# Kernel optimization log

Hardware: AMD Instinct MI355X
Metric: run time of the kernel (lower is better)

Reference implementation:

```python
import jax, jax.numpy as jnp
import numpy as np

D_MODEL, D_HEAD, N_HEAD, PERIOD = 1024, 64, 16, 30
B, T1, T2 = 2, 2048, 2048


def setup_inputs() -> dict:
    key = jax.random.key(0)
    ks = jax.random.split(key, 7)
    s_in = 1.0 / np.sqrt(D_MODEL)
    s_out = 1.0 / np.sqrt(N_HEAD * D_HEAD)
    return {
        "x": jax.random.normal(ks[0], (B, T1, D_MODEL), dtype=jnp.float32),
        "context": jax.random.normal(ks[1], (B, T2, D_MODEL), dtype=jnp.float32),
        "Wq": jax.random.uniform(ks[2], (N_HEAD * D_HEAD, D_MODEL), jnp.float32, -s_in, s_in),
        "Wk": jax.random.uniform(ks[3], (N_HEAD * D_HEAD, D_MODEL), jnp.float32, -s_in, s_in),
        "Wv": jax.random.uniform(ks[4], (N_HEAD * D_HEAD, D_MODEL), jnp.float32, -s_in, s_in),
        "Wo": jax.random.uniform(ks[5], (D_MODEL, N_HEAD * D_HEAD), jnp.float32, -s_out, s_out),
        "bo": jax.random.uniform(ks[6], (D_MODEL,), jnp.float32, -s_out, s_out),
    }


def reference(x, context, Wq, Wk, Wv, Wo, bo):
    Bx, T1x, _ = x.shape
    T2x = context.shape[1]
    scale = 1.0 / np.sqrt(D_HEAD).astype(np.float32)
    # projections (torch Linear: y = x @ W^T)
    q = (x @ Wq.T).reshape(Bx, T1x, N_HEAD, D_HEAD)
    k = (context @ Wk.T).reshape(Bx, T2x, N_HEAD, D_HEAD)
    v = (context @ Wv.T).reshape(Bx, T2x, N_HEAD, D_HEAD)
    # attention scores [B, H, T1, T2]
    scores = jnp.einsum('bihd,bjhd->bhij', q, k) * scale
    # ALiBi-style periodic distance bias
    dist = jnp.abs(jnp.arange(T1x)[:, None] - jnp.arange(T2x)[None, :])  # [T1,T2]
    bias = -(dist // PERIOD).astype(jnp.float32)                          # [T1,T2]
    head_scale = jnp.power(2.0, -jnp.arange(1, N_HEAD + 1, dtype=jnp.float32))
    biased = scores + bias[None, None, :, :] * head_scale[None, :, None, None]
    attn = jax.nn.softmax(biased, axis=-1)
    out = jnp.einsum('bhij,bjhd->bihd', attn, v).reshape(Bx, T1x, N_HEAD * D_HEAD)
    # output projection; dropout is identity in eval mode
    return out @ Wo.T + bo
```

## Files before the change

kernel.cpp:

```cpp
#include <hip/hip_runtime.h>
#include <hip/hip_fp16.h>

typedef _Float16 f16;
typedef __attribute__((ext_vector_type(8))) _Float16 f16x8;
typedef __attribute__((ext_vector_type(4))) _Float16 f16x4;
typedef __attribute__((ext_vector_type(2))) __fp16 fp16x2;
typedef __attribute__((ext_vector_type(4))) float f32x4;

#define DM 1024
#define NH 16
#define DH 64
#define TT 2048
#define LOG2E 1.4426950408889634f
#define QSCALE 0.18033688f

__device__ __forceinline__ void gl16(const void* g, void* l) {
  __builtin_amdgcn_global_load_lds((const __attribute__((address_space(1))) void*)g,
                                   (__attribute__((address_space(3))) void*)l, 16, 0, 0);
}

__global__ __launch_bounds__(256) void cvt_all(const float* __restrict__ x, const float* __restrict__ cx,
                                               const float* __restrict__ wq, const float* __restrict__ wk,
                                               const float* __restrict__ wv, const float* __restrict__ wo,
                                               f16* __restrict__ xb, f16* __restrict__ cb,
                                               f16* __restrict__ wqb, f16* __restrict__ wkb,
                                               f16* __restrict__ wvb, f16* __restrict__ wob) {
  int idx = blockIdx.x * 256 + threadIdx.x;
  int stride = gridDim.x * 256;
  for (int i = idx; i < 3145728; i += stride) {
    const float* src; f16* dst; int off; float s = 1.0f;
    if (i < 2097152) {
      if (i < 1048576) { src = x; dst = xb; off = i; }
      else { src = cx; dst = cb; off = i - 1048576; }
    } else {
      int j = i - 2097152;
      int wsel = j >> 18;
      off = j & 262143;
      if (wsel == 0) { src = wq; dst = wqb; s = QSCALE; }
      else if (wsel == 1) { src = wk; dst = wkb; }
      else if (wsel == 2) { src = wv; dst = wvb; }
      else { src = wo; dst = wob; }
    }
    float4 v = reinterpret_cast<const float4*>(src)[off];
    f16x4 o = { (f16)(v.x * s), (f16)(v.y * s), (f16)(v.z * s), (f16)(v.w * s) };
    reinterpret_cast<f16x4*>(dst)[off] = o;
  }
}

__global__ __launch_bounds__(256) void fbgen(f16* __restrict__ FB) {
  int i = blockIdx.x;
  int j0 = threadIdx.x * 8;
  f16x8 v;
#pragma unroll
  for (int e = 0; e < 8; e++) {
    int d = i - (j0 + e); d = (d < 0) ? -d : d;
    v[e] = (f16)(d / 30);
  }
  *reinterpret_cast<f16x8*>(&FB[(size_t)i * TT + j0]) = v;
}

__device__ __forceinline__ void gemm_mainloop(const f16* __restrict__ A, const f16* __restrict__ W,
                                              int bm, int bn, f16 (*As)[4096], f16 (*Bs)[4096],
                                              f32x4 (&acc)[4][4]) {
  int t = threadIdx.x;
  int w = t >> 6;
  int lane = t & 63, lr = lane & 15, g = lane >> 4;
  int wr = w >> 1, wc = w & 1;
  int scol = ((t & 3) ^ ((t >> 3) & 3)) * 8;
  const f16* a0 = A + (size_t)(bm + (t >> 2)) * DM + scol;
  const f16* b0 = W + (size_t)(bn + (t >> 2)) * DM + scol;
  int wo = w * 512;
  int szg = ((lr >> 1) & 3) << 4;

  auto STG = [&](int bufi, int kt) {
    gl16(a0 + kt, As[bufi] + wo);
    gl16(a0 + kt + (size_t)64 * DM, As[bufi] + 2048 + wo);
    gl16(b0 + kt, Bs[bufi] + wo);
    gl16(b0 + kt + (size_t)64 * DM, Bs[bufi] + 2048 + wo);
  };

  STG(0, 0);
  __syncthreads();
  int buf = 0;
  for (int kt = 0; kt < DM; kt += 32) {
    if (kt + 32 < DM) STG(buf ^ 1, kt + 32);
    const char* Ab = (const char*)As[buf];
    const char* Bb = (const char*)Bs[buf];
    f16x8 af[4], bf[4];
#pragma unroll
    for (int mi = 0; mi < 4; mi++) {
      int row = wr * 64 + mi * 16 + lr;
      af[mi] = *reinterpret_cast<const f16x8*>(Ab + row * 64 + ((g << 4) ^ szg));
    }
#pragma unroll
    for (int ni = 0; ni < 4; ni++) {
      int row = wc * 64 + ni * 16 + lr;
      bf[ni] = *reinterpret_cast<const f16x8*>(Bb + row * 64 + ((g << 4) ^ szg));
    }
    __builtin_amdgcn_s_setprio(1);
#pragma unroll
    for (int mi = 0; mi < 4; mi++)
#pragma unroll
      for (int ni = 0; ni < 4; ni++)
        acc[mi][ni] = __builtin_amdgcn_mfma_f32_16x16x32_f16(af[mi], bf[ni], acc[mi][ni], 0, 0, 0);
    __builtin_amdgcn_s_setprio(0);
    __syncthreads();
    buf ^= 1;
  }
}

__global__ __launch_bounds__(256) void qkv_gemm(const f16* __restrict__ xb, const f16* __restrict__ cb,
                                                const f16* __restrict__ wq, const f16* __restrict__ wk,
                                                const f16* __restrict__ wv,
                                                f16* __restrict__ Qo, f16* __restrict__ Ko,
                                                f16* __restrict__ Vt) {
  __shared__ f16 As[2][4096];
  __shared__ f16 Bs[2][4096];
  int gid = blockIdx.x >> 8;
  int bid = blockIdx.x & 255;
  int bm = (bid >> 3) * 128, bn = (bid & 7) * 128;
  const f16* A = (gid == 0) ? xb : cb;
  const f16* W = (gid == 0) ? wq : ((gid == 1) ? wk : wv);
  f32x4 acc[4][4] = {};
  gemm_mainloop(A, W, bm, bn, As, Bs, acc);

  int t = threadIdx.x, w = t >> 6, lane = t & 63, lr = lane & 15, g = lane >> 4;
  int wr = w >> 1, wc = w & 1;
  if (gid < 2) {
    f16* out = (gid == 0) ? Qo : Ko;
#pragma unroll
    for (int mi = 0; mi < 4; mi++) {
      int m0 = bm + wr * 64 + mi * 16 + 4 * g;
      int b = m0 >> 11, i0 = m0 & 2047;
#pragma unroll
      for (int ni = 0; ni < 4; ni++) {
        int n = bn + wc * 64 + ni * 16 + lr;
        int h = n >> 6, d = n & 63;
        size_t base = (((size_t)(b * NH + h)) * TT + i0) * DH + d;
#pragma unroll
        for (int r = 0; r < 4; r++)
          out[base + (size_t)r * DH] = (f16)acc[mi][ni][r];
      }
    }
  } else {
#pragma unroll
    for (int mi = 0; mi < 4; mi++) {
      int m0 = bm + wr * 64 + mi * 16 + 4 * g;
      int b = m0 >> 11, j0 = m0 & 2047;
#pragma unroll
      for (int ni = 0; ni < 4; ni++) {
        int n = bn + wc * 64 + ni * 16 + lr;
        int h = n >> 6, d = n & 63;
        f16x4 pk = { (f16)acc[mi][ni][0], (f16)acc[mi][ni][1],
                     (f16)acc[mi][ni][2], (f16)acc[mi][ni][3] };
        *reinterpret_cast<f16x4*>(&Vt[(((size_t)(b * NH + h)) * DH + d) * TT + j0]) = pk;
      }
    }
  }
}

__global__ __launch_bounds__(256) void out_gemm(const f16* __restrict__ Ob, const f16* __restrict__ wo,
                                                const float* __restrict__ bo, float* __restrict__ Y) {
  __shared__ f16 As[2][4096];
  __shared__ f16 Bs[2][4096];
  int bid = blockIdx.x;
  int bm = (bid >> 3) * 128, bn = (bid & 7) * 128;
  f32x4 acc[4][4] = {};
  gemm_mainloop(Ob, wo, bm, bn, As, Bs, acc);
  int t = threadIdx.x, w = t >> 6, lane = t & 63, lr = lane & 15, g = lane >> 4;
  int wr = w >> 1, wc = w & 1;
#pragma unroll
  for (int mi = 0; mi < 4; mi++) {
    int m0 = bm + wr * 64 + mi * 16 + 4 * g;
#pragma unroll
    for (int ni = 0; ni < 4; ni++) {
      int n = bn + wc * 64 + ni * 16 + lr;
      float bias = bo[n];
#pragma unroll
      for (int r = 0; r < 4; r++)
        Y[(size_t)(m0 + r) * DM + n] = acc[mi][ni][r] + bias;
    }
  }
}

__global__ __launch_bounds__(256, 4) void attn_kernel(const f16* __restrict__ Q, const f16* __restrict__ K,
                                                      const f16* __restrict__ V, const f16* __restrict__ FB,
                                                      f16* __restrict__ O) {
  __shared__ f16 KV[2][8192];
  int o = blockIdx.x;
  int bid = (((o & 7) << 2) + (o >> 8)) * 32 + ((o >> 3) & 31);
  int qt = bid & 31, bh = bid >> 5, h = bh & 15, b = bh >> 4;
  int t = threadIdx.x, w = t >> 6, lane = t & 63, lr = lane & 15, g = lane >> 4;
  int qw = qt * 64 + w * 16;
  int qi = qw + lr;

  const f16* qrow = Q + ((size_t)bh * TT + qi) * DH + g * 8;
  f16x8 qf0 = *reinterpret_cast<const f16x8*>(qrow);
  f16x8 qf1 = *reinterpret_cast<const f16x8*>(qrow + 32);

  const float nc2 = -exp2f(-(float)(h + 1)) * LOG2E;
  f32x4 rsv = { 0.f, 0.f, 0.f, 0.f };
  f32x4 oacc[4] = {};

  const f16* fbrow = FB + (size_t)qi * TT + (g << 3);

  int srow = w * 8 + (lane >> 3);
  int gr = lane & 7;
  int sw = gr ^ ((srow & 3) | ((srow & 8) >> 1));
  const f16* ksrc = K + ((size_t)bh * TT + srow) * DH + sw * 8;
  const f16* vsrc = V + ((size_t)bh * DH + srow) * TT + sw * 8;
  int wo = w * 512;

  auto STG = [&](int bufi, int kv0) {
    f16* base = KV[bufi];
    gl16(ksrc + (size_t)kv0 * DH, base + wo);
    gl16(ksrc + (size_t)(kv0 + 32) * DH, base + 2048 + wo);
    gl16(vsrc + kv0, base + 4096 + wo);
    gl16(vsrc + (size_t)32 * TT + kv0, base + 6144 + wo);
  };

  int jp = ((lr >> 2) << 3) + (lr & 3);
  int szk = ((lr & 3) | (((lr >> 2) & 1) << 2)) << 4;
  int szv = ((lr & 3) | ((lr & 8) >> 1)) << 4;

  STG(0, 0);
  __syncthreads();
  int buf = 0;

  for (int kv0 = 0; kv0 < TT; kv0 += 64) {
    if (kv0 + 64 < TT) STG(buf ^ 1, kv0 + 64);
    f16x8 fbv0 = *reinterpret_cast<const f16x8*>(fbrow + kv0);
    f16x8 fbv1 = *reinterpret_cast<const f16x8*>(fbrow + kv0 + 32);

    const char* Kb = (const char*)KV[buf];
    const char* Vb = Kb + 8192;

    f32x4 sv[4];
    __builtin_amdgcn_s_setprio(1);
#pragma unroll
    for (int ct = 0; ct < 4; ct++) {
      int jrow = jp + ((ct >> 1) << 5) + ((ct & 1) << 2);
      const char* krow = Kb + jrow * 128;
      f16x8 kb0 = *reinterpret_cast<const f16x8*>(krow + ((g << 4) ^ szk));
      f16x8 kb1 = *reinterpret_cast<const f16x8*>(krow + (((g + 4) << 4) ^ szk));
      f32x4 z = {0.f, 0.f, 0.f, 0.f};
      z = __builtin_amdgcn_mfma_f32_16x16x32_f16(kb0, qf0, z, 0, 0, 0);
      z = __builtin_amdgcn_mfma_f32_16x16x32_f16(kb1, qf1, z, 0, 0, 0);
      sv[ct] = z;
    }
    __builtin_amdgcn_s_setprio(0);

#pragma unroll
    for (int ct = 0; ct < 4; ct++) {
      int e0 = (ct & 1) << 2;
      f32x4 p;
#pragma unroll
      for (int r = 0; r < 4; r++) {
        float fbf = (ct < 2) ? (float)fbv0[e0 + r] : (float)fbv1[e0 + r];
        float sx = fmaf(fbf, nc2, sv[ct][r]);
        p[r] = __builtin_amdgcn_exp2f(sx);
      }
      sv[ct] = p;
      rsv += p;
    }

#pragma unroll
    for (int ks = 0; ks < 2; ks++) {
      union { f16x8 v; fp16x2 hh[4]; } pu;
      pu.hh[0] = __builtin_amdgcn_cvt_pkrtz(sv[2 * ks][0], sv[2 * ks][1]);
      pu.hh[1] = __builtin_amdgcn_cvt_pkrtz(sv[2 * ks][2], sv[2 * ks][3]);
      pu.hh[2] = __builtin_amdgcn_cvt_pkrtz(sv[2 * ks + 1][0], sv[2 * ks + 1][1]);
      pu.hh[3] = __builtin_amdgcn_cvt_pkrtz(sv[2 * ks + 1][2], sv[2 * ks + 1][3]);
      __builtin_amdgcn_s_setprio(1);
#pragma unroll
      for (int dt = 0; dt < 4; dt++) {
        int vr = dt * 16 + lr;
        f16x8 va = *reinterpret_cast<const f16x8*>(Vb + vr * 128 + ((((ks * 4 + g)) << 4) ^ szv));
        oacc[dt] = __builtin_amdgcn_mfma_f32_16x16x32_f16(va, pu.v, oacc[dt], 0, 0, 0);
      }
      __builtin_amdgcn_s_setprio(0);
    }
    __syncthreads();
    buf ^= 1;
  }

  float lsum = (rsv[0] + rsv[1]) + (rsv[2] + rsv[3]);
  lsum += __shfl_xor(lsum, 16, 64);
  lsum += __shfl_xor(lsum, 32, 64);
  float inv = __builtin_amdgcn_rcpf(lsum);
  size_t ob = ((size_t)b * TT + qi) * DM + h * DH + (g << 2);
#pragma unroll
  for (int dt = 0; dt < 4; dt++) {
    f16x4 o4 = { (f16)(oacc[dt][0] * inv), (f16)(oacc[dt][1] * inv),
                 (f16)(oacc[dt][2] * inv), (f16)(oacc[dt][3] * inv) };
    *reinterpret_cast<f16x4*>(&O[ob + dt * 16]) = o4;
  }
}

extern "C" void kernel_launch(void* const* d_in, const int* in_sizes, int n_in,
                              void* d_out, int out_size, void* d_ws, size_t ws_size,
                              hipStream_t stream) {
  const float* x  = (const float*)d_in[0];
  const float* cx = (const float*)d_in[1];
  const float* Wq = (const float*)d_in[2];
  const float* Wk = (const float*)d_in[3];
  const float* Wv = (const float*)d_in[4];
  const float* Wo = (const float*)d_in[5];
  const float* bo = (const float*)d_in[6];
  float* Y = (float*)d_out;

  const size_t NTOK = (size_t)2 * TT;
  f16* p = (f16*)d_ws;
  f16* xb  = p; p += NTOK * DM;
  f16* cb  = p; p += NTOK * DM;
  f16* wqb = p; p += (size_t)DM * DM;
  f16* wkb = p; p += (size_t)DM * DM;
  f16* wvb = p; p += (size_t)DM * DM;
  f16* wob = p; p += (size_t)DM * DM;
  f16* Qb  = p; p += NTOK * DM;
  f16* Kb  = p; p += NTOK * DM;
  f16* Vtb = p; p += NTOK * DM;
  f16* Ob  = p; p += NTOK * DM;
  f16* FBt = xb;

  cvt_all<<<2048, 256, 0, stream>>>(x, cx, Wq, Wk, Wv, Wo, xb, cb, wqb, wkb, wvb, wob);
  qkv_gemm<<<768, 256, 0, stream>>>(xb, cb, wqb, wkb, wvb, Qb, Kb, Vtb);
  fbgen<<<TT, 256, 0, stream>>>(FBt);
  attn_kernel<<<1024, 256, 0, stream>>>(Qb, Kb, Vtb, FBt, Ob);
  out_gemm<<<256, 256, 0, stream>>>(Ob, wob, bo, Y);
}
```

Before: 136.9 us.

## Switch attention to 32x32x16 MFMA with 128-query tiles per block

Rewrites the attention kernel to use 32x32x16 MFMA instructions instead of 16x16x32. Each wave now owns 32 queries and each block 128, so the grid is halved and every staged K/V tile is reused by twice as many queries. The LDS read swizzle and the staging row mapping are redone to match the new fragment layout, and launch bounds drop to 2 blocks per CU. Larger accumulators raise register pressure and lower occupancy, and the fewer blocks may fill the CUs less evenly.

```diff
diff --git a/kernel.cpp b/kernel.cpp
--- a/kernel.cpp
+++ b/kernel.cpp
@@ -6,6 +6,7 @@
 typedef __attribute__((ext_vector_type(4))) _Float16 f16x4;
 typedef __attribute__((ext_vector_type(2))) __fp16 fp16x2;
 typedef __attribute__((ext_vector_type(4))) float f32x4;
+typedef __attribute__((ext_vector_type(16))) float f32x16;
 
 #define DM 1024
 #define NH 16
@@ -183,32 +184,36 @@
   }
 }
 
-__global__ __launch_bounds__(256, 4) void attn_kernel(const f16* __restrict__ Q, const f16* __restrict__ K,
+__global__ __launch_bounds__(256, 2) void attn_kernel(const f16* __restrict__ Q, const f16* __restrict__ K,
                                                       const f16* __restrict__ V, const f16* __restrict__ FB,
                                                       f16* __restrict__ O) {
   __shared__ f16 KV[2][8192];
   int o = blockIdx.x;
-  int bid = (((o & 7) << 2) + (o >> 8)) * 32 + ((o >> 3) & 31);
-  int qt = bid & 31, bh = bid >> 5, h = bh & 15, b = bh >> 4;
-  int t = threadIdx.x, w = t >> 6, lane = t & 63, lr = lane & 15, g = lane >> 4;
-  int qw = qt * 64 + w * 16;
-  int qi = qw + lr;
-
-  const f16* qrow = Q + ((size_t)bh * TT + qi) * DH + g * 8;
-  f16x8 qf0 = *reinterpret_cast<const f16x8*>(qrow);
-  f16x8 qf1 = *reinterpret_cast<const f16x8*>(qrow + 32);
+  int x = o & 7, idx = o >> 3;
+  int bh = 4 * x + (idx >> 4), qt = idx & 15;
+  int h = bh & 15, b = bh >> 4;
+  int t = threadIdx.x, w = t >> 6, lane = t & 63;
+  int col = lane & 31, hi = lane >> 5;
+  int qi = qt * 128 + w * 32 + col;
+
+  const f16* qp = Q + ((size_t)bh * TT + qi) * DH + hi * 8;
+  f16x8 qf[4];
+  qf[0] = *reinterpret_cast<const f16x8*>(qp);
+  qf[1] = *reinterpret_cast<const f16x8*>(qp + 16);
+  qf[2] = *reinterpret_cast<const f16x8*>(qp + 32);
+  qf[3] = *reinterpret_cast<const f16x8*>(qp + 48);
 
   const float nc2 = -exp2f(-(float)(h + 1)) * LOG2E;
-  f32x4 rsv = { 0.f, 0.f, 0.f, 0.f };
-  f32x4 oacc[4] = {};
-
-  const f16* fbrow = FB + (size_t)qi * TT + (g << 3);
-
-  int srow = w * 8 + (lane >> 3);
-  int gr = lane & 7;
-  int sw = gr ^ ((srow & 3) | ((srow & 8) >> 1));
-  const f16* ksrc = K + ((size_t)bh * TT + srow) * DH + sw * 8;
-  const f16* vsrc = V + ((size_t)bh * DH + srow) * TT + sw * 8;
+  const f16* fbrow = FB + (size_t)qi * TT + hi * 8;
+
+  float lsum = 0.f;
+  f32x16 oacc[2] = {};
+
+  int trow = t >> 3;
+  int graw = (t & 7) ^ (trow & 7);
+  int j0 = 16 * ((t >> 7) & 1) + 8 * ((t >> 5) & 1) + 4 * ((t >> 6) & 1) + ((t >> 3) & 3);
+  const f16* ksrc = K + ((size_t)bh * TT + j0) * DH + graw * 8;
+  const f16* vsrc = V + ((size_t)bh * DH + trow) * TT + graw * 8;
   int wo = w * 512;
 
   auto STG = [&](int bufi, int kv0) {
@@ -219,9 +224,10 @@
     gl16(vsrc + (size_t)32 * TT + kv0, base + 6144 + wo);
   };
 
-  int jp = ((lr >> 2) << 3) + (lr & 3);
-  int szk = ((lr & 3) | (((lr >> 2) & 1) << 2)) << 4;
-  int szv = ((lr & 3) | ((lr & 8) >> 1)) << 4;
+  int rbase = col * 128;
+  int gsw[4];
+#pragma unroll
+  for (int s = 0; s < 4; s++) gsw[s] = (((2 * s + hi) ^ (lane & 7)) << 4);
 
   STG(0, 0);
   __syncthreads();
@@ -229,72 +235,70 @@
 
   for (int kv0 = 0; kv0 < TT; kv0 += 64) {
     if (kv0 + 64 < TT) STG(buf ^ 1, kv0 + 64);
-    f16x8 fbv0 = *reinterpret_cast<const f16x8*>(fbrow + kv0);
-    f16x8 fbv1 = *reinterpret_cast<const f16x8*>(fbrow + kv0 + 32);
+    f16x8 fbv[4];
+    fbv[0] = *reinterpret_cast<const f16x8*>(fbrow + kv0);
+    fbv[1] = *reinterpret_cast<const f16x8*>(fbrow + kv0 + 16);
+    fbv[2] = *reinterpret_cast<const f16x8*>(fbrow + kv0 + 32);
+    fbv[3] = *reinterpret_cast<const f16x8*>(fbrow + kv0 + 48);
 
     const char* Kb = (const char*)KV[buf];
     const char* Vb = Kb + 8192;
 
-    f32x4 sv[4];
+    f32x16 sj[2] = {};
     __builtin_amdgcn_s_setprio(1);
 #pragma unroll
-    for (int ct = 0; ct < 4; ct++) {
-      int jrow = jp + ((ct >> 1) << 5) + ((ct & 1) << 2);
-      const char* krow = Kb + jrow * 128;
-      f16x8 kb0 = *reinterpret_cast<const f16x8*>(krow + ((g << 4) ^ szk));
-      f16x8 kb1 = *reinterpret_cast<const f16x8*>(krow + (((g + 4) << 4) ^ szk));
-      f32x4 z = {0.f, 0.f, 0.f, 0.f};
-      z = __builtin_amdgcn_mfma_f32_16x16x32_f16(kb0, qf0, z, 0, 0, 0);
-      z = __builtin_amdgcn_mfma_f32_16x16x32_f16(kb1, qf1, z, 0, 0, 0);
-      sv[ct] = z;
+    for (int s = 0; s < 4; s++) {
+      f16x8 ka = *reinterpret_cast<const f16x8*>(Kb + rbase + gsw[s]);
+      f16x8 kb = *reinterpret_cast<const f16x8*>(Kb + 4096 + rbase + gsw[s]);
+      sj[0] = __builtin_amdgcn_mfma_f32_32x32x16_f16(ka, qf[s], sj[0], 0, 0, 0);
+      sj[1] = __builtin_amdgcn_mfma_f32_32x32x16_f16(kb, qf[s], sj[1], 0, 0, 0);
     }
     __builtin_amdgcn_s_setprio(0);
 
-#pragma unroll
-    for (int ct = 0; ct < 4; ct++) {
-      int e0 = (ct & 1) << 2;
-      f32x4 p;
-#pragma unroll
-      for (int r = 0; r < 4; r++) {
-        float fbf = (ct < 2) ? (float)fbv0[e0 + r] : (float)fbv1[e0 + r];
-        float sx = fmaf(fbf, nc2, sv[ct][r]);
-        p[r] = __builtin_amdgcn_exp2f(sx);
+    f16x8 pb[4];
+#pragma unroll
+    for (int s = 0; s < 4; s++) {
+      const int jb = s >> 1, ro = 8 * (s & 1);
+      float p[8];
+#pragma unroll
+      for (int e = 0; e < 8; e++) {
+        float sx = fmaf((float)fbv[s][e], nc2, sj[jb][ro + e]);
+        p[e] = __builtin_amdgcn_exp2f(sx);
       }
-      sv[ct] = p;
-      rsv += p;
-    }
-
-#pragma unroll
-    for (int ks = 0; ks < 2; ks++) {
+      lsum += ((p[0] + p[1]) + (p[2] + p[3])) + ((p[4] + p[5]) + (p[6] + p[7]));
       union { f16x8 v; fp16x2 hh[4]; } pu;
-      pu.hh[0] = __builtin_amdgcn_cvt_pkrtz(sv[2 * ks][0], sv[2 * ks][1]);
-      pu.hh[1] = __builtin_amdgcn_cvt_pkrtz(sv[2 * ks][2], sv[2 * ks][3]);
-      pu.hh[2] = __builtin_amdgcn_cvt_pkrtz(sv[2 * ks + 1][0], sv[2 * ks + 1][1]);
-      pu.hh[3] = __builtin_amdgcn_cvt_pkrtz(sv[2 * ks + 1][2], sv[2 * ks + 1][3]);
-      __builtin_amdgcn_s_setprio(1);
-#pragma unroll
-      for (int dt = 0; dt < 4; dt++) {
-        int vr = dt * 16 + lr;
-        f16x8 va = *reinterpret_cast<const f16x8*>(Vb + vr * 128 + ((((ks * 4 + g)) << 4) ^ szv));
-        oacc[dt] = __builtin_amdgcn_mfma_f32_16x16x32_f16(va, pu.v, oacc[dt], 0, 0, 0);
-      }
-      __builtin_amdgcn_s_setprio(0);
-    }
+      pu.hh[0] = __builtin_amdgcn_cvt_pkrtz(p[0], p[1]);
+      pu.hh[1] = __builtin_amdgcn_cvt_pkrtz(p[2], p[3]);
+      pu.hh[2] = __builtin_amdgcn_cvt_pkrtz(p[4], p[5]);
+      pu.hh[3] = __builtin_amdgcn_cvt_pkrtz(p[6], p[7]);
+      pb[s] = pu.v;
+    }
+
+    __builtin_amdgcn_s_setprio(1);
+#pragma unroll
+    for (int s = 0; s < 4; s++) {
+      f16x8 va0 = *reinterpret_cast<const f16x8*>(Vb + rbase + gsw[s]);
+      f16x8 va1 = *reinterpret_cast<const f16x8*>(Vb + 4096 + rbase + gsw[s]);
+      oacc[0] = __builtin_amdgcn_mfma_f32_32x32x16_f16(va0, pb[s], oacc[0], 0, 0, 0);
+      oacc[1] = __builtin_amdgcn_mfma_f32_32x32x16_f16(va1, pb[s], oacc[1], 0, 0, 0);
+    }
+    __builtin_amdgcn_s_setprio(0);
     __syncthreads();
     buf ^= 1;
   }
 
-  float lsum = (rsv[0] + rsv[1]) + (rsv[2] + rsv[3]);
-  lsum += __shfl_xor(lsum, 16, 64);
   lsum += __shfl_xor(lsum, 32, 64);
   float inv = __builtin_amdgcn_rcpf(lsum);
-  size_t ob = ((size_t)b * TT + qi) * DM + h * DH + (g << 2);
-#pragma unroll
-  for (int dt = 0; dt < 4; dt++) {
-    f16x4 o4 = { (f16)(oacc[dt][0] * inv), (f16)(oacc[dt][1] * inv),
-                 (f16)(oacc[dt][2] * inv), (f16)(oacc[dt][3] * inv) };
-    *reinterpret_cast<f16x4*>(&O[ob + dt * 16]) = o4;
-  }
+
+  size_t ob = ((size_t)b * TT + qi) * DM + h * DH + 4 * hi;
+#pragma unroll
+  for (int db = 0; db < 2; db++)
+#pragma unroll
+    for (int k = 0; k < 4; k++) {
+      f16x4 o4 = { (f16)(oacc[db][4 * k] * inv),     (f16)(oacc[db][4 * k + 1] * inv),
+                   (f16)(oacc[db][4 * k + 2] * inv), (f16)(oacc[db][4 * k + 3] * inv) };
+      *reinterpret_cast<f16x4*>(&O[ob + 32 * db + 8 * k]) = o4;
+    }
 }
 
 extern "C" void kernel_launch(void* const* d_in, const int* in_sizes, int n_in,
@@ -326,6 +330,6 @@
   cvt_all<<<2048, 256, 0, stream>>>(x, cx, Wq, Wk, Wv, Wo, xb, cb, wqb, wkb, wvb, wob);
   qkv_gemm<<<768, 256, 0, stream>>>(xb, cb, wqb, wkb, wvb, Qb, Kb, Vtb);
   fbgen<<<TT, 256, 0, stream>>>(FBt);
-  attn_kernel<<<1024, 256, 0, stream>>>(Qb, Kb, Vtb, FBt, Ob);
+  attn_kernel<<<512, 256, 0, stream>>>(Qb, Kb, Vtb, FBt, Ob);
   out_gemm<<<256, 256, 0, stream>>>(Ob, wob, bo, Y);
 }
```

Result: faster. 132.7 us (-3.1%).
